# Kernel tuning notes

Hardware: AMD Instinct MI355X
Metric: run time of the kernel (lower is better)

The kernel has to match this reference:

```python
import jax, jax.numpy as jnp
import numpy as np

NUM_HEADS = 16
HEAD_DIM = 64
D_MODEL = 1024
B, L = 8, 4096


def _relative_position_encoding(seq_len, dim):
    positions = jnp.arange(seq_len, dtype=jnp.float32)[:, None]
    div_term = jnp.exp(jnp.arange(0, dim, 2, dtype=jnp.float32) * (-(np.log(10000.0) / dim)))
    ang = positions * div_term  # [L, dim//2]
    pe = jnp.zeros((seq_len, dim), dtype=jnp.float32)
    pe = pe.at[:, 0::2].set(jnp.sin(ang))
    pe = pe.at[:, 1::2].set(jnp.cos(ang))
    return pe


def setup_inputs() -> dict:
    key = jax.random.key(0)
    k1, k2, k3 = jax.random.split(key, 3)
    x = jax.random.normal(k1, (B, L, D_MODEL), dtype=jnp.float32)
    w_qkv = jax.random.normal(k2, (D_MODEL, 3 * NUM_HEADS * HEAD_DIM), dtype=jnp.float32) * (1.0 / np.sqrt(D_MODEL))
    b_qkv = jnp.zeros((3 * NUM_HEADS * HEAD_DIM,), dtype=jnp.float32)
    w_out = jax.random.normal(k3, (NUM_HEADS * HEAD_DIM, D_MODEL), dtype=jnp.float32) * (1.0 / np.sqrt(NUM_HEADS * HEAD_DIM))
    b_out = jnp.zeros((D_MODEL,), dtype=jnp.float32)
    return {"x": x, "w_qkv": w_qkv, "b_qkv": b_qkv, "w_out": w_out, "b_out": b_out}


def reference(x, w_qkv, b_qkv, w_out, b_out):
    Bq, Lq, _ = x.shape
    qkv = x @ w_qkv + b_qkv                              # [B, L, 3*H*Dh]
    qkv = qkv.reshape(Bq, Lq, NUM_HEADS, 3 * HEAD_DIM)   # [B, L, H, 3*Dh]
    q, k, v = jnp.split(qkv, 3, axis=-1)                 # each [B, L, H, Dh]
    pos_enc = _relative_position_encoding(Lq, HEAD_DIM)  # [L, Dh]
    k = k + pos_enc[None, :, None, :]
    scale = jnp.sqrt(jnp.float32(HEAD_DIM))
    # NOTE: faithful to source -- contraction over head_dim with batch dims (B, L):
    # attention matrix is [B, L, H, H] (across heads, not sequence).
    attn = jnp.einsum('blhd,bl gd->blhg'.replace(' ', ''), q, k) / scale  # [B, L, H, H]
    attn = jax.nn.softmax(attn, axis=-1)
    out = jnp.einsum('blhg,blgd->blhd', attn, v)          # [B, L, H, Dh]
    out = out.reshape(Bq, Lq, NUM_HEADS * HEAD_DIM)
    return out @ w_out + b_out
```

## Files before the change

kernel.cpp:

```cpp
#include <hip/hip_runtime.h>
#include <hip/hip_bf16.h>
#include <cstdint>
#include <cstddef>

#define NH   16
#define DHD  64
#define DM   1024
#define BSZ  8
#define SEQ  4096
#define NTOK (BSZ*SEQ)
#define NQKV (3*NH*DHD)

typedef __attribute__((ext_vector_type(8))) __bf16 bf16x8;
typedef __attribute__((ext_vector_type(4))) float  floatx4;
typedef __attribute__((ext_vector_type(4))) _Float16 f16x4;

static __device__ __forceinline__ unsigned short f2bf(float f) {
    unsigned int u = __float_as_uint(f);
    u += 0x7fffu + ((u >> 16) & 1u);
    return (unsigned short)(u >> 16);
}
static __device__ __forceinline__ float bf2f(unsigned int us) {
    return __uint_as_float(us << 16);
}
static __device__ __forceinline__ unsigned short f2h(float f) {
    _Float16 h = (_Float16)f;
    return __builtin_bit_cast(unsigned short, h);
}
static __device__ __forceinline__ void load_lds16(const void* g, void* l) {
    __builtin_amdgcn_global_load_lds((__attribute__((address_space(1))) void*)g,
                                     (__attribute__((address_space(3))) void*)l,
                                     16, 0, 0);
}

__global__ __launch_bounds__(256) void k_cast_bf16(const float* __restrict__ in,
                                                   unsigned short* __restrict__ out, int n4) {
    int i = blockIdx.x * 256 + threadIdx.x;
    if (i >= n4) return;
    float4 v = ((const float4*)in)[i];
    ushort4 o;
    o.x = f2bf(v.x); o.y = f2bf(v.y); o.z = f2bf(v.z); o.w = f2bf(v.w);
    ((ushort4*)out)[i] = o;
}

template<int R, int C>
__global__ __launch_bounds__(256) void k_transpose_cast(const float* __restrict__ in,
                                                        unsigned short* __restrict__ out) {
    __shared__ float tile[32][33];
    int tx = threadIdx.x, ty = threadIdx.y;
    int col = blockIdx.x * 32 + tx;
#pragma unroll
    for (int k = 0; k < 4; k++) {
        int row = blockIdx.y * 32 + ty + k * 8;
        tile[ty + k * 8][tx] = in[(size_t)row * C + col];
    }
    __syncthreads();
#pragma unroll
    for (int k = 0; k < 4; k++) {
        int ocol = blockIdx.x * 32 + ty + k * 8;
        int orow = blockIdx.y * 32 + tx;
        out[(size_t)ocol * R + orow] = f2bf(tile[tx][ty + k * 8]);
    }
}

__global__ __launch_bounds__(256) void k_pe(float* __restrict__ pe) {
    int t = blockIdx.x * 256 + threadIdx.x;
    int l = t >> 5, i = t & 31;
    float dv = expf(-0.14391156831212787f * (float)(2 * i));
    float ang = (float)l * dv;
    pe[l * 64 + 2 * i]     = sinf(ang);
    pe[l * 64 + 2 * i + 1] = cosf(ang);
}

template<int N, int EPI>
__global__ __launch_bounds__(256) void k_gemm(const unsigned short* __restrict__ A,
                                              const unsigned short* __restrict__ BT,
                                              const float* __restrict__ bias,
                                              const float* __restrict__ pe,
                                              void* __restrict__ Cout) {
    constexpr int K = 1024;
    __shared__ __align__(16) short lds[8704];
    short* As = lds;
    short* Bs = lds + 4096;

    int tid  = threadIdx.x;
    int lane = tid & 63;
    int wid  = tid >> 6;
    int m0 = blockIdx.y * 128;
    int n0 = blockIdx.x * 128;
    int wr = wid >> 1, wc = wid & 1;
    int l15 = lane & 15;
    int quad = lane >> 4;
    int kq  = quad * 8;

    floatx4 acc[4][4];
#pragma unroll
    for (int i = 0; i < 4; i++)
#pragma unroll
        for (int j = 0; j < 4; j++) acc[i][j] = (floatx4){0.f, 0.f, 0.f, 0.f};

    int ci0 = wid * 128 + lane;
    int ci1 = ci0 + 64;
    const unsigned short* pa0 = A  + (size_t)(m0 + (ci0 >> 2)) * K + (ci0 & 3) * 8;
    const unsigned short* pa1 = A  + (size_t)(m0 + (ci1 >> 2)) * K + (ci1 & 3) * 8;
    const unsigned short* pb0 = BT + (size_t)(n0 + (ci0 >> 2)) * K + (ci0 & 3) * 8;
    const unsigned short* pb1 = BT + (size_t)(n0 + (ci1 >> 2)) * K + (ci1 & 3) * 8;
    short* la0 = As + ci0 * 8;
    short* la1 = As + ci1 * 8;
    short* lb0 = Bs + ci0 * 8;
    short* lb1 = Bs + ci1 * 8;

    for (int kb = 0; kb < K; kb += 32) {
        __syncthreads();
        load_lds16(pa0 + kb, la0);
        load_lds16(pa1 + kb, la1);
        load_lds16(pb0 + kb, lb0);
        load_lds16(pb1 + kb, lb1);
        __syncthreads();

        bf16x8 aF[4], bF[4];
#pragma unroll
        for (int i = 0; i < 4; i++)
            aF[i] = *(const bf16x8*)&As[(wr * 64 + i * 16 + l15) * 32 + kq];
#pragma unroll
        for (int j = 0; j < 4; j++)
            bF[j] = *(const bf16x8*)&Bs[(wc * 64 + j * 16 + l15) * 32 + kq];
#pragma unroll
        for (int i = 0; i < 4; i++)
#pragma unroll
            for (int j = 0; j < 4; j++)
                acc[i][j] = __builtin_amdgcn_mfma_f32_16x16x32_bf16(aF[i], bF[j], acc[i][j], 0, 0, 0);
    }

    if (EPI == 1) {
        short* T = lds;
        __syncthreads();
#pragma unroll
        for (int p = 0; p < 2; p++) {
            if (wr == p) {
#pragma unroll
                for (int j = 0; j < 4; j++) {
                    int col = n0 + wc * 64 + j * 16 + l15;
                    float bv = bias[col];
                    int h = col / 192, rc = col - h * 192;
                    int csw = (wc * 64 + j * 16 + l15) ^ (quad << 3);
#pragma unroll
                    for (int i = 0; i < 4; i++) {
#pragma unroll
                        for (int r = 0; r < 4; r++) {
                            int rl = i * 16 + quad * 4 + r;
                            int row = m0 + p * 64 + rl;
                            float v = acc[i][j][r] + bv;
                            if (rc < 64)       v *= 0.125f;
                            else if (rc < 128) v += pe[(row & (SEQ - 1)) * 64 + (rc - 64)];
                            T[rl * 136 + csw] = (short)f2bf(v);
                        }
                    }
                }
            }
            __syncthreads();
            {
                int rl = tid >> 2, coff = (tid & 3) * 32;
                int sw = ((rl >> 2) & 3) * 8;
                unsigned short* dst = (unsigned short*)Cout + (size_t)(m0 + p * 64 + rl) * N + n0 + coff;
#pragma unroll
                for (int k = 0; k < 4; k++) {
                    uint4 u = *(const uint4*)&T[rl * 136 + ((coff + k * 8) ^ sw)];
                    *(uint4*)(dst + k * 8) = u;
                }
            }
            __syncthreads();
        }
    } else {
        int rbase = quad * 4;
#pragma unroll
        for (int j = 0; j < 4; j++) {
            int col = n0 + wc * 64 + j * 16 + l15;
            float bv = bias[col];
#pragma unroll
            for (int i = 0; i < 4; i++) {
#pragma unroll
                for (int r = 0; r < 4; r++) {
                    int row = m0 + wr * 64 + i * 16 + rbase + r;
                    ((float*)Cout)[(size_t)row * N + col] = acc[i][j][r] + bv;
                }
            }
        }
    }
}

__global__ __launch_bounds__(256) void k_attn(const unsigned short* __restrict__ qkv,
                                              unsigned short* __restrict__ aout) {
    __shared__ __align__(16) unsigned short lds[4][2752];
    int tid = threadIdx.x, wid = tid >> 6, lane = tid & 63;
    unsigned short* VT = lds[wid];
    unsigned short* PL = VT + 1280;
    unsigned short* OL = PL + 320;
    int t = blockIdx.x * 4 + wid;
    int l15 = lane & 15, q = lane >> 4;

    const unsigned short* rowp = qkv + (size_t)t * NQKV + l15 * 192 + q * 8;

    bf16x8 aQ0 = *(const bf16x8*)(rowp);
    bf16x8 bK0 = *(const bf16x8*)(rowp + 64);
    bf16x8 aQ1 = *(const bf16x8*)(rowp + 32);
    bf16x8 bK1 = *(const bf16x8*)(rowp + 96);
    uint4  v0  = *(const uint4*)(rowp + 128);
    uint4  v1  = *(const uint4*)(rowp + 160);

    floatx4 S = {0.f, 0.f, 0.f, 0.f};
    S = __builtin_amdgcn_mfma_f32_16x16x32_bf16(aQ0, bK0, S, 0, 0, 0);
    S = __builtin_amdgcn_mfma_f32_16x16x32_bf16(aQ1, bK1, S, 0, 0, 0);

    {
        unsigned int w0[4] = {v0.x, v0.y, v0.z, v0.w};
        unsigned int w1[4] = {v1.x, v1.y, v1.z, v1.w};
#pragma unroll
        for (int i = 0; i < 4; i++) {
            int d = q * 8 + 2 * i;
            VT[(d)      * 20 + l15] = f2h(bf2f(w0[i] & 0xffff));
            VT[(d + 1)  * 20 + l15] = f2h(bf2f(w0[i] >> 16));
            VT[(d + 32) * 20 + l15] = f2h(bf2f(w1[i] & 0xffff));
            VT[(d + 33) * 20 + l15] = f2h(bf2f(w1[i] >> 16));
        }
    }

    float e0, e1, e2, e3, i0, i1, i2, i3;
    {
        float m0 = S[0], m1 = S[1], m2 = S[2], m3 = S[3];
#pragma unroll
        for (int d = 1; d < 16; d <<= 1) {
            m0 = fmaxf(m0, __shfl_xor(m0, d));
            m1 = fmaxf(m1, __shfl_xor(m1, d));
            m2 = fmaxf(m2, __shfl_xor(m2, d));
            m3 = fmaxf(m3, __shfl_xor(m3, d));
        }
        e0 = __expf(S[0] - m0); e1 = __expf(S[1] - m1);
        e2 = __expf(S[2] - m2); e3 = __expf(S[3] - m3);
        float s0 = e0, s1 = e1, s2 = e2, s3 = e3;
#pragma unroll
        for (int d = 1; d < 16; d <<= 1) {
            s0 += __shfl_xor(s0, d); s1 += __shfl_xor(s1, d);
            s2 += __shfl_xor(s2, d); s3 += __shfl_xor(s3, d);
        }
        i0 = 1.f / s0; i1 = 1.f / s1; i2 = 1.f / s2; i3 = 1.f / s3;
    }
    PL[(q * 4 + 0) * 20 + l15] = f2h(e0);
    PL[(q * 4 + 1) * 20 + l15] = f2h(e1);
    PL[(q * 4 + 2) * 20 + l15] = f2h(e2);
    PL[(q * 4 + 3) * 20 + l15] = f2h(e3);

    f16x4 aP = *(const f16x4*)&PL[l15 * 20 + q * 4];
    floatx4 O[4];
#pragma unroll
    for (int c = 0; c < 4; c++) {
        f16x4 bV = *(const f16x4*)&VT[(c * 16 + l15) * 20 + q * 4];
        O[c] = __builtin_amdgcn_mfma_f32_16x16x16f16(aP, bV, (floatx4){0.f, 0.f, 0.f, 0.f}, 0, 0, 0);
    }

    float inv[4] = {i0, i1, i2, i3};
#pragma unroll
    for (int c = 0; c < 4; c++)
#pragma unroll
        for (int r = 0; r < 4; r++)
            OL[(q * 4 + r) * 72 + c * 16 + l15] = f2bf(O[c][r] * inv[r]);

    int h2 = lane >> 2, a = lane & 3;
    uint4 o0 = *(const uint4*)&OL[h2 * 72 + a * 16];
    uint4 o1 = *(const uint4*)&OL[h2 * 72 + a * 16 + 8];
    uint4* dst = (uint4*)&aout[(size_t)t * DM + lane * 16];
    dst[0] = o0;
    dst[1] = o1;
}

extern "C" void kernel_launch(void* const* d_in, const int* in_sizes, int n_in,
                              void* d_out, int out_size, void* d_ws, size_t ws_size,
                              hipStream_t stream) {
    const float* x     = (const float*)d_in[0];
    const float* w_qkv = (const float*)d_in[1];
    const float* b_qkv = (const float*)d_in[2];
    const float* w_out = (const float*)d_in[3];
    const float* b_out = (const float*)d_in[4];
    float* out = (float*)d_out;

    char* ws = (char*)d_ws;
    float*          pe    = (float*)ws;
    unsigned short* wqkvT = (unsigned short*)(ws + (1u << 20));
    unsigned short* woutT = (unsigned short*)(ws + (1u << 20) + 6291456u);
    unsigned short* xbf   = (unsigned short*)(ws + (1u << 20) + 6291456u + 2097152u);
    unsigned short* qkv   = (unsigned short*)(ws + (1u << 20) + 6291456u + 2097152u + 67108864u);
    unsigned short* aout  = xbf;

    k_cast_bf16<<<(NTOK * DM / 4 + 255) / 256, 256, 0, stream>>>(x, xbf, NTOK * DM / 4);
    k_transpose_cast<1024, 3072><<<dim3(96, 32), dim3(32, 8), 0, stream>>>(w_qkv, wqkvT);
    k_transpose_cast<1024, 1024><<<dim3(32, 32), dim3(32, 8), 0, stream>>>(w_out, woutT);
    k_pe<<<512, 256, 0, stream>>>(pe);

    k_gemm<NQKV, 1><<<dim3(NQKV / 128, NTOK / 128), 256, 0, stream>>>(xbf, wqkvT, b_qkv, pe, qkv);
    k_attn<<<NTOK / 4, 256, 0, stream>>>(qkv, aout);
    k_gemm<DM, 0><<<dim3(DM / 128, NTOK / 128), 256, 0, stream>>>(aout, woutT, b_out, nullptr, out);
}
```

Baseline: 791.9 us.

## Load two K-slices per barrier pair and stage full epilogue tile at once

The GEMM main loop now loads 64 K-elements (two 32-wide slices into separate LDS buffers) per pair of barriers, halving the number of __syncthreads in the K loop. The EPI==1 epilogue writes the whole 128x128 tile to LDS in one pass instead of two halves, removing extra barriers, and each thread then stores 64 contiguous columns. LDS usage doubles to about 34 KB, which may reduce occupancy. Loads still are not overlapped with compute.

```diff
diff --git a/kernel.cpp b/kernel.cpp
--- a/kernel.cpp
+++ b/kernel.cpp
@@ -79,9 +79,11 @@
                                               const float* __restrict__ pe,
                                               void* __restrict__ Cout) {
     constexpr int K = 1024;
-    __shared__ __align__(16) short lds[8704];
-    short* As = lds;
-    short* Bs = lds + 4096;
+    __shared__ __align__(16) short lds[17408];
+    short* As0 = lds;
+    short* Bs0 = lds + 4096;
+    short* As1 = lds + 8192;
+    short* Bs1 = lds + 12288;
 
     int tid  = threadIdx.x;
     int lane = tid & 63;
@@ -105,71 +107,73 @@
     const unsigned short* pa1 = A  + (size_t)(m0 + (ci1 >> 2)) * K + (ci1 & 3) * 8;
     const unsigned short* pb0 = BT + (size_t)(n0 + (ci0 >> 2)) * K + (ci0 & 3) * 8;
     const unsigned short* pb1 = BT + (size_t)(n0 + (ci1 >> 2)) * K + (ci1 & 3) * 8;
-    short* la0 = As + ci0 * 8;
-    short* la1 = As + ci1 * 8;
-    short* lb0 = Bs + ci0 * 8;
-    short* lb1 = Bs + ci1 * 8;
-
-    for (int kb = 0; kb < K; kb += 32) {
+    short* la0 = As0 + ci0 * 8;
+    short* la1 = As0 + ci1 * 8;
+    short* lb0 = Bs0 + ci0 * 8;
+    short* lb1 = Bs0 + ci1 * 8;
+
+    auto compute32 = [&](const short* Asb, const short* Bsb) {
+        bf16x8 aF[4], bF[4];
+#pragma unroll
+        for (int i = 0; i < 4; i++)
+            aF[i] = *(const bf16x8*)&Asb[(wr * 64 + i * 16 + l15) * 32 + kq];
+#pragma unroll
+        for (int j = 0; j < 4; j++)
+            bF[j] = *(const bf16x8*)&Bsb[(wc * 64 + j * 16 + l15) * 32 + kq];
+#pragma unroll
+        for (int i = 0; i < 4; i++)
+#pragma unroll
+            for (int j = 0; j < 4; j++)
+                acc[i][j] = __builtin_amdgcn_mfma_f32_16x16x32_bf16(aF[i], bF[j], acc[i][j], 0, 0, 0);
+    };
+
+    for (int kb = 0; kb < K; kb += 64) {
         __syncthreads();
         load_lds16(pa0 + kb, la0);
         load_lds16(pa1 + kb, la1);
         load_lds16(pb0 + kb, lb0);
         load_lds16(pb1 + kb, lb1);
+        load_lds16(pa0 + kb + 32, la0 + 8192);
+        load_lds16(pa1 + kb + 32, la1 + 8192);
+        load_lds16(pb0 + kb + 32, lb0 + 8192);
+        load_lds16(pb1 + kb + 32, lb1 + 8192);
         __syncthreads();
-
-        bf16x8 aF[4], bF[4];
-#pragma unroll
-        for (int i = 0; i < 4; i++)
-            aF[i] = *(const bf16x8*)&As[(wr * 64 + i * 16 + l15) * 32 + kq];
-#pragma unroll
-        for (int j = 0; j < 4; j++)
-            bF[j] = *(const bf16x8*)&Bs[(wc * 64 + j * 16 + l15) * 32 + kq];
-#pragma unroll
-        for (int i = 0; i < 4; i++)
-#pragma unroll
-            for (int j = 0; j < 4; j++)
-                acc[i][j] = __builtin_amdgcn_mfma_f32_16x16x32_bf16(aF[i], bF[j], acc[i][j], 0, 0, 0);
+        compute32(As0, Bs0);
+        compute32(As1, Bs1);
     }
 
     if (EPI == 1) {
         short* T = lds;
         __syncthreads();
 #pragma unroll
-        for (int p = 0; p < 2; p++) {
-            if (wr == p) {
-#pragma unroll
-                for (int j = 0; j < 4; j++) {
-                    int col = n0 + wc * 64 + j * 16 + l15;
-                    float bv = bias[col];
-                    int h = col / 192, rc = col - h * 192;
-                    int csw = (wc * 64 + j * 16 + l15) ^ (quad << 3);
-#pragma unroll
-                    for (int i = 0; i < 4; i++) {
-#pragma unroll
-                        for (int r = 0; r < 4; r++) {
-                            int rl = i * 16 + quad * 4 + r;
-                            int row = m0 + p * 64 + rl;
-                            float v = acc[i][j][r] + bv;
-                            if (rc < 64)       v *= 0.125f;
-                            else if (rc < 128) v += pe[(row & (SEQ - 1)) * 64 + (rc - 64)];
-                            T[rl * 136 + csw] = (short)f2bf(v);
-                        }
-                    }
+        for (int j = 0; j < 4; j++) {
+            int col = n0 + wc * 64 + j * 16 + l15;
+            float bv = bias[col];
+            int h = col / 192, rc = col - h * 192;
+            int csw = (wc * 64 + j * 16 + l15) ^ (quad << 3);
+#pragma unroll
+            for (int i = 0; i < 4; i++) {
+#pragma unroll
+                for (int r = 0; r < 4; r++) {
+                    int rl = wr * 64 + i * 16 + quad * 4 + r;
+                    int row = m0 + rl;
+                    float v = acc[i][j][r] + bv;
+                    if (rc < 64)       v *= 0.125f;
+                    else if (rc < 128) v += pe[(row & (SEQ - 1)) * 64 + (rc - 64)];
+                    T[rl * 136 + csw] = (short)f2bf(v);
                 }
             }
-            __syncthreads();
-            {
-                int rl = tid >> 2, coff = (tid & 3) * 32;
-                int sw = ((rl >> 2) & 3) * 8;
-                unsigned short* dst = (unsigned short*)Cout + (size_t)(m0 + p * 64 + rl) * N + n0 + coff;
-#pragma unroll
-                for (int k = 0; k < 4; k++) {
-                    uint4 u = *(const uint4*)&T[rl * 136 + ((coff + k * 8) ^ sw)];
-                    *(uint4*)(dst + k * 8) = u;
-                }
+        }
+        __syncthreads();
+        {
+            int row = tid >> 1, coff = (tid & 1) * 64;
+            int sw = ((row >> 2) & 3) * 8;
+            unsigned short* dst = (unsigned short*)Cout + (size_t)(m0 + row) * N + n0 + coff;
+#pragma unroll
+            for (int k = 0; k < 8; k++) {
+                uint4 u = *(const uint4*)&T[row * 136 + ((coff + k * 8) ^ sw)];
+                *(uint4*)(dst + k * 8) = u;
             }
-            __syncthreads();
         }
     } else {
         int rbase = quad * 4;
```

Result: no change. 782.9 us (-1.1%).
